# Optimization experiments

Hardware: AMD Instinct MI355X
Metric: run time of the kernel (lower is better)

Reference implementation:

```python
import jax, jax.numpy as jnp
import numpy as np

N_NODES = 500_000
N_EDGES = 16_000_000
N_LAYERS = 49
ALPHA = 0.3  # GCN2Conv alpha; beta = 1.0 (no theta/layer given)

# per-layer activation applied AFTER the conv (layer index 0-based)
_LEAKY = {1, 11, 21, 31, 41}
_SIG = {4, 14, 24, 34, 44}


def setup_inputs() -> dict:
    key = jax.random.key(0)
    k1, k2, k3 = jax.random.split(key, 3)
    x = jax.random.normal(k1, (N_NODES, 1), dtype=jnp.float32)
    adj = jax.random.randint(k2, (2, N_EDGES), 0, N_NODES, dtype=jnp.int64)
    # 49 scalar (1x1) layer weights
    w = jax.random.normal(k3, (N_LAYERS,), dtype=jnp.float32) * 0.1
    return {"input": x, "w": w, "adj": adj}


def _gcn_norm(adj, n):
    # add self-loops, symmetric normalization D^-1/2 (A+I) D^-1/2
    loops = jnp.arange(n, dtype=adj.dtype)
    src = jnp.concatenate([adj[0], loops])
    dst = jnp.concatenate([adj[1], loops])
    deg = jax.ops.segment_sum(jnp.ones(src.shape[0], jnp.float32), dst, num_segments=n)
    dis = 1.0 / jnp.sqrt(deg)  # deg >= 1 due to self-loops
    ew = dis[src] * dis[dst]
    return src, dst, ew


def reference(input, w, adj):
    n = input.shape[0]
    x0 = input.astype(jnp.float32)
    src, dst, ew = _gcn_norm(adj, n)
    ewc = ew[:, None]  # [E+N, 1]

    def gcn2(x, wl):
        h = jax.ops.segment_sum(ewc * x[src], dst, num_segments=n)  # A_hat @ x
        comb = (1.0 - ALPHA) * h + ALPHA * x0                       # residual mix
        return comb * wl                                            # 1x1 weight, beta=1

    x = x0
    for i in range(N_LAYERS):
        y = gcn2(x, w[i])
        if i == 0:
            x = y  # no activation after gcn1
        elif i == N_LAYERS - 1:
            x = n * jax.nn.sigmoid(y)  # CustomSigmoid: len(x) * sigmoid(x)
        elif i in _LEAKY:
            x = jax.nn.leaky_relu(y, 0.01)
        elif i in _SIG:
            x = jax.nn.sigmoid(y)
        else:
            x = jax.nn.relu(y)
        # dropout(p=0.0) is identity
    return jnp.squeeze(x, 1).astype(jnp.int64)
```

## Files before the change

### kernel.cpp

```cpp
#include <hip/hip_runtime.h>
#include <math.h>

#define NN 500000
#define NE 16000000
#define NBKT 1954
#define PB 40960
#define NPB_BLOCKS ((NE + PB - 1) / PB)

__global__ __launch_bounds__(256) void hist_kernel(const int4* __restrict__ dst4,
                                                   int* __restrict__ bcnt) {
    __shared__ int lh[NBKT];
    for (int i = threadIdx.x; i < NBKT; i += 256) lh[i] = 0;
    __syncthreads();
    long base4 = (long)blockIdx.x * (PB / 4);
    for (int k = 0; k < PB / 4; k += 256) {
        long i4 = base4 + k + threadIdx.x;
        if (i4 < NE / 4) {
            int4 d = dst4[i4];
            atomicAdd(&lh[d.x >> 8], 1);
            atomicAdd(&lh[d.y >> 8], 1);
            atomicAdd(&lh[d.z >> 8], 1);
            atomicAdd(&lh[d.w >> 8], 1);
        }
    }
    __syncthreads();
    for (int i = threadIdx.x; i < NBKT; i += 256) {
        int c = lh[i];
        if (c) atomicAdd(&bcnt[i], c);
    }
}

__global__ __launch_bounds__(256) void scan_buckets(int* __restrict__ bcnt,
                                                    int* __restrict__ bbase) {
    __shared__ int sh[256];
    __shared__ int carry_sh;
    if (threadIdx.x == 0) carry_sh = 0;
    __syncthreads();
    for (int base = 0; base < NBKT; base += 256) {
        int i = base + threadIdx.x;
        int v = (i < NBKT) ? bcnt[i] : 0;
        sh[threadIdx.x] = v;
        __syncthreads();
        for (int off = 1; off < 256; off <<= 1) {
            int t = (threadIdx.x >= off) ? sh[threadIdx.x - off] : 0;
            __syncthreads();
            sh[threadIdx.x] += t;
            __syncthreads();
        }
        int incl = sh[threadIdx.x];
        int c = carry_sh;
        __syncthreads();
        if (i < NBKT) {
            int ex = c + incl - v;
            bbase[i] = ex;
            bcnt[i] = ex;
        }
        if (threadIdx.x == 255) carry_sh = c + incl;
        __syncthreads();
    }
    if (threadIdx.x == 0) bbase[NBKT] = NE;
}

__global__ __launch_bounds__(256) void partition_kernel(const int* __restrict__ src,
                                                        const int* __restrict__ dst,
                                                        int* __restrict__ bcur,
                                                        int* __restrict__ ebuf) {
    __shared__ int lh[NBKT];
    for (int i = threadIdx.x; i < NBKT; i += 256) lh[i] = 0;
    __syncthreads();
    long base = (long)blockIdx.x * PB;
    for (int k = 0; k < PB; k += 256) {
        long e = base + k + threadIdx.x;
        if (e < NE) atomicAdd(&lh[dst[e] >> 8], 1);
    }
    __syncthreads();
    for (int i = threadIdx.x; i < NBKT; i += 256) {
        int c = lh[i];
        if (c) lh[i] = atomicAdd(&bcur[i], c);
    }
    __syncthreads();
    for (int k = 0; k < PB; k += 256) {
        long e = base + k + threadIdx.x;
        if (e < NE) {
            int d = dst[e];
            int pos = atomicAdd(&lh[d >> 8], 1);
            ebuf[pos] = ((d & 255) << 19) | src[e];
        }
    }
}

__global__ __launch_bounds__(256) void bucket_deg(const int* __restrict__ bbase,
                                                  const int* __restrict__ ebuf,
                                                  float* __restrict__ dis) {
    __shared__ int cnt[256];
    int b = blockIdx.x;
    int ebase = bbase[b];
    int nb = bbase[b + 1] - ebase;
    cnt[threadIdx.x] = 0;
    __syncthreads();
    for (int i = threadIdx.x; i < nb; i += 256)
        atomicAdd(&cnt[ebuf[ebase + i] >> 19], 1);
    __syncthreads();
    int v = b * 256 + threadIdx.x;
    if (v < NN) dis[v] = rsqrtf((float)(cnt[threadIdx.x] + 1));
}

__global__ void init_z(const float* __restrict__ x0, const float* __restrict__ dis,
                       float* __restrict__ z) {
    int i = blockIdx.x * 256 + threadIdx.x;
    if (i < NN) z[i] = x0[i] * dis[i];
}

__global__ __launch_bounds__(256) void layer_kernel(
        const int* __restrict__ bbase, const int* __restrict__ ebuf,
        const float* __restrict__ zin, const float* __restrict__ dis,
        const float* __restrict__ x0, const float* __restrict__ w,
        int li, int act, float* __restrict__ zout, int* __restrict__ out) {
    __shared__ float h[256];
    int b = blockIdx.x;
    int ebase = bbase[b];
    int nb = bbase[b + 1] - ebase;
    h[threadIdx.x] = 0.f;
    __syncthreads();
    for (int i = threadIdx.x; i < nb; i += 256) {
        int e = ebuf[ebase + i];
        atomicAdd(&h[e >> 19], zin[e & 0x7FFFF]);
    }
    __syncthreads();
    int v = b * 256 + threadIdx.x;
    if (v >= NN) return;
    float s = h[threadIdx.x] + zin[v];
    float hh = dis[v] * s;
    float comb = 0.7f * hh + 0.3f * x0[v];
    float y = comb * w[li];
    if (act == 4) {
        float sg = 1.f / (1.f + expf(-y));
        out[v] = (int)(500000.f * sg);
        return;
    }
    float r;
    if (act == 0)      r = y;
    else if (act == 1) r = fmaxf(y, 0.f);
    else if (act == 2) r = (y > 0.f) ? y : 0.01f * y;
    else               r = 1.f / (1.f + expf(-y));
    zout[v] = dis[v] * r;
}

extern "C" void kernel_launch(void* const* d_in, const int* in_sizes, int n_in,
                              void* d_out, int out_size, void* d_ws, size_t ws_size,
                              hipStream_t stream) {
    const float* x0  = (const float*)d_in[0];
    const float* w   = (const float*)d_in[1];
    const int*   adj = (const int*)d_in[2];
    const int*   src = adj;
    const int*   dst = adj + NE;
    int* out = (int*)d_out;

    uintptr_t p = (uintptr_t)d_ws;
    auto alloc = [&](size_t bytes) -> void* {
        p = (p + 255) & ~(uintptr_t)255;
        void* r = (void*)p;
        p += bytes;
        return r;
    };
    float* dis   = (float*)alloc((size_t)NN * 4);
    float* z0    = (float*)alloc((size_t)NN * 4);
    float* z1    = (float*)alloc((size_t)NN * 4);
    int*   bcnt  = (int*)alloc((size_t)NBKT * 4);
    int*   bbase = (int*)alloc((size_t)(NBKT + 1) * 4);
    int*   csr   = (int*)alloc((size_t)NE * 4);
    (void)ws_size;

    hipMemsetAsync(bcnt, 0, (size_t)NBKT * 4, stream);

    hist_kernel<<<NPB_BLOCKS, 256, 0, stream>>>((const int4*)dst, bcnt);
    scan_buckets<<<1, 256, 0, stream>>>(bcnt, bbase);
    partition_kernel<<<NPB_BLOCKS, 256, 0, stream>>>(src, dst, bcnt, csr);
    bucket_deg<<<NBKT, 256, 0, stream>>>(bbase, csr, dis);
    init_z<<<(NN + 255) / 256, 256, 0, stream>>>(x0, dis, z0);

    float* zbuf[2] = {z0, z1};
    for (int i = 0; i < 49; i++) {
        int act;
        if (i == 0)            act = 0;
        else if (i == 48)      act = 4;
        else if (i % 10 == 1)  act = 2;
        else if (i % 10 == 4)  act = 3;
        else                   act = 1;
        layer_kernel<<<NBKT, 256, 0, stream>>>(bbase, csr, zbuf[i & 1], dis, x0, w,
                                               i, act, zbuf[(i + 1) & 1], out);
    }
}
```

Measured before the change: 4.941 ms.

## Two-level partition of edges by dst supertile and src cell for gather locality

Edges are now first partitioned by destination into 8192-node supertiles, then within each supertile sorted by source cell (1024-node groups), so gathers of zin within a block hit nearby addresses. Each layer is split into an accumulate kernel, where 16 chunks per supertile reduce into an 8192-entry shared histogram and flush via global atomics, and a finalize kernel that applies the activation and clears the accumulator. This aims to improve cache locality of the random src gathers and to use larger shared tiles. In exchange it adds an extra sort pass, global float atomics, and a second launch per layer.

```diff
diff --git a/kernel.cpp b/kernel.cpp
--- a/kernel.cpp
+++ b/kernel.cpp
@@ -3,42 +3,131 @@
 
 #define NN 500000
 #define NE 16000000
-#define NBKT 1954
-#define PB 40960
-#define NPB_BLOCKS ((NE + PB - 1) / PB)
-
-__global__ __launch_bounds__(256) void hist_kernel(const int4* __restrict__ dst4,
-                                                   int* __restrict__ bcnt) {
-    __shared__ int lh[NBKT];
-    for (int i = threadIdx.x; i < NBKT; i += 256) lh[i] = 0;
-    __syncthreads();
-    long base4 = (long)blockIdx.x * (PB / 4);
-    for (int k = 0; k < PB / 4; k += 256) {
+#define ST 62
+#define STB 8192
+#define NG 489
+#define PBA 16384
+#define NBA ((NE/4 + PBA/4 - 1) / (PBA/4))
+#define SUBB 16
+#define NBB (ST * SUBB)
+#define CHUNKS 16
+#define NBACC (ST * CHUNKS)
+
+__global__ __launch_bounds__(256) void histA(const int4* __restrict__ dst4,
+                                             int* __restrict__ bcntA) {
+    __shared__ int lh[ST];
+    if (threadIdx.x < ST) lh[threadIdx.x] = 0;
+    __syncthreads();
+    long base4 = (long)blockIdx.x * (PBA / 4);
+    for (int k = 0; k < PBA / 4; k += 256) {
         long i4 = base4 + k + threadIdx.x;
         if (i4 < NE / 4) {
             int4 d = dst4[i4];
-            atomicAdd(&lh[d.x >> 8], 1);
-            atomicAdd(&lh[d.y >> 8], 1);
-            atomicAdd(&lh[d.z >> 8], 1);
-            atomicAdd(&lh[d.w >> 8], 1);
-        }
-    }
-    __syncthreads();
-    for (int i = threadIdx.x; i < NBKT; i += 256) {
-        int c = lh[i];
-        if (c) atomicAdd(&bcnt[i], c);
-    }
-}
-
-__global__ __launch_bounds__(256) void scan_buckets(int* __restrict__ bcnt,
-                                                    int* __restrict__ bbase) {
+            atomicAdd(&lh[d.x >> 13], 1);
+            atomicAdd(&lh[d.y >> 13], 1);
+            atomicAdd(&lh[d.z >> 13], 1);
+            atomicAdd(&lh[d.w >> 13], 1);
+        }
+    }
+    __syncthreads();
+    if (threadIdx.x < ST) {
+        int c = lh[threadIdx.x];
+        if (c) atomicAdd(&bcntA[threadIdx.x], c);
+    }
+}
+
+__global__ void scanA(const int* __restrict__ bcntA, int* __restrict__ regBase,
+                      int* __restrict__ curA) {
+    int i = threadIdx.x;
+    int v = (i < ST) ? bcntA[i] : 0;
+    int incl = v;
+    for (int off = 1; off < 64; off <<= 1) {
+        int t = __shfl_up(incl, off);
+        if (i >= off) incl += t;
+    }
+    if (i < ST) { regBase[i] = incl - v; curA[i] = incl - v; }
+    if (i == 63) regBase[ST] = incl;
+}
+
+__global__ __launch_bounds__(256) void scatterA(const int4* __restrict__ src4,
+                                                const int4* __restrict__ dst4,
+                                                int* __restrict__ curA,
+                                                unsigned* __restrict__ tmp) {
+    __shared__ int lh[ST];
+    if (threadIdx.x < ST) lh[threadIdx.x] = 0;
+    __syncthreads();
+    long base4 = (long)blockIdx.x * (PBA / 4);
+    for (int k = 0; k < PBA / 4; k += 256) {
+        long i4 = base4 + k + threadIdx.x;
+        if (i4 < NE / 4) {
+            int4 d = dst4[i4];
+            atomicAdd(&lh[d.x >> 13], 1);
+            atomicAdd(&lh[d.y >> 13], 1);
+            atomicAdd(&lh[d.z >> 13], 1);
+            atomicAdd(&lh[d.w >> 13], 1);
+        }
+    }
+    __syncthreads();
+    if (threadIdx.x < ST) {
+        int c = lh[threadIdx.x];
+        if (c) lh[threadIdx.x] = atomicAdd(&curA[threadIdx.x], c);
+    }
+    __syncthreads();
+    for (int k = 0; k < PBA / 4; k += 256) {
+        long i4 = base4 + k + threadIdx.x;
+        if (i4 < NE / 4) {
+            int4 d = dst4[i4];
+            int4 s = src4[i4];
+            int p;
+            p = atomicAdd(&lh[d.x >> 13], 1); tmp[p] = ((unsigned)(d.x & 8191) << 19) | (unsigned)s.x;
+            p = atomicAdd(&lh[d.y >> 13], 1); tmp[p] = ((unsigned)(d.y & 8191) << 19) | (unsigned)s.y;
+            p = atomicAdd(&lh[d.z >> 13], 1); tmp[p] = ((unsigned)(d.z & 8191) << 19) | (unsigned)s.z;
+            p = atomicAdd(&lh[d.w >> 13], 1); tmp[p] = ((unsigned)(d.w & 8191) << 19) | (unsigned)s.w;
+        }
+    }
+}
+
+__global__ __launch_bounds__(256) void histB(const unsigned* __restrict__ tmp,
+                                             const int* __restrict__ regBase,
+                                             int* __restrict__ cellCnt,
+                                             int* __restrict__ deg) {
+    __shared__ int gh[NG];
+    __shared__ int dh[STB];
+    int st = blockIdx.x >> 4, sb = blockIdx.x & 15;
+    int base = regBase[st];
+    int len = regBase[st + 1] - base;
+    int beg = base + (int)((long)len * sb / SUBB);
+    int end = base + (int)((long)len * (sb + 1) / SUBB);
+    for (int i = threadIdx.x; i < NG; i += 256) gh[i] = 0;
+    for (int i = threadIdx.x; i < STB; i += 256) dh[i] = 0;
+    __syncthreads();
+    for (int i = beg + threadIdx.x; i < end; i += 256) {
+        unsigned e = tmp[i];
+        atomicAdd(&gh[(e & 0x7FFFFu) >> 10], 1);
+        atomicAdd(&dh[e >> 19], 1);
+    }
+    __syncthreads();
+    for (int i = threadIdx.x; i < NG; i += 256) {
+        int c = gh[i];
+        if (c) atomicAdd(&cellCnt[st * NG + i], c);
+    }
+    for (int i = threadIdx.x; i < STB; i += 256) {
+        int c = dh[i];
+        if (c) atomicAdd(&deg[st * STB + i], c);
+    }
+}
+
+__global__ __launch_bounds__(256) void scanB(const int* __restrict__ regBase,
+                                             const int* __restrict__ cellCnt,
+                                             int* __restrict__ cellCur) {
     __shared__ int sh[256];
     __shared__ int carry_sh;
-    if (threadIdx.x == 0) carry_sh = 0;
-    __syncthreads();
-    for (int base = 0; base < NBKT; base += 256) {
+    int st = blockIdx.x;
+    if (threadIdx.x == 0) carry_sh = regBase[st];
+    __syncthreads();
+    for (int base = 0; base < NG; base += 256) {
         int i = base + threadIdx.x;
-        int v = (i < NBKT) ? bcnt[i] : 0;
+        int v = (i < NG) ? cellCnt[st * NG + i] : 0;
         sh[threadIdx.x] = v;
         __syncthreads();
         for (int off = 1; off < 256; off <<= 1) {
@@ -50,86 +139,86 @@
         int incl = sh[threadIdx.x];
         int c = carry_sh;
         __syncthreads();
-        if (i < NBKT) {
-            int ex = c + incl - v;
-            bbase[i] = ex;
-            bcnt[i] = ex;
-        }
+        if (i < NG) cellCur[st * NG + i] = c + incl - v;
         if (threadIdx.x == 255) carry_sh = c + incl;
         __syncthreads();
     }
-    if (threadIdx.x == 0) bbase[NBKT] = NE;
-}
-
-__global__ __launch_bounds__(256) void partition_kernel(const int* __restrict__ src,
-                                                        const int* __restrict__ dst,
-                                                        int* __restrict__ bcur,
-                                                        int* __restrict__ ebuf) {
-    __shared__ int lh[NBKT];
-    for (int i = threadIdx.x; i < NBKT; i += 256) lh[i] = 0;
-    __syncthreads();
-    long base = (long)blockIdx.x * PB;
-    for (int k = 0; k < PB; k += 256) {
-        long e = base + k + threadIdx.x;
-        if (e < NE) atomicAdd(&lh[dst[e] >> 8], 1);
-    }
-    __syncthreads();
-    for (int i = threadIdx.x; i < NBKT; i += 256) {
-        int c = lh[i];
-        if (c) lh[i] = atomicAdd(&bcur[i], c);
-    }
-    __syncthreads();
-    for (int k = 0; k < PB; k += 256) {
-        long e = base + k + threadIdx.x;
-        if (e < NE) {
-            int d = dst[e];
-            int pos = atomicAdd(&lh[d >> 8], 1);
-            ebuf[pos] = ((d & 255) << 19) | src[e];
-        }
-    }
-}
-
-__global__ __launch_bounds__(256) void bucket_deg(const int* __restrict__ bbase,
-                                                  const int* __restrict__ ebuf,
-                                                  float* __restrict__ dis) {
-    __shared__ int cnt[256];
-    int b = blockIdx.x;
-    int ebase = bbase[b];
-    int nb = bbase[b + 1] - ebase;
-    cnt[threadIdx.x] = 0;
-    __syncthreads();
-    for (int i = threadIdx.x; i < nb; i += 256)
-        atomicAdd(&cnt[ebuf[ebase + i] >> 19], 1);
-    __syncthreads();
-    int v = b * 256 + threadIdx.x;
-    if (v < NN) dis[v] = rsqrtf((float)(cnt[threadIdx.x] + 1));
-}
-
-__global__ void init_z(const float* __restrict__ x0, const float* __restrict__ dis,
-                       float* __restrict__ z) {
-    int i = blockIdx.x * 256 + threadIdx.x;
-    if (i < NN) z[i] = x0[i] * dis[i];
-}
-
-__global__ __launch_bounds__(256) void layer_kernel(
-        const int* __restrict__ bbase, const int* __restrict__ ebuf,
-        const float* __restrict__ zin, const float* __restrict__ dis,
-        const float* __restrict__ x0, const float* __restrict__ w,
-        int li, int act, float* __restrict__ zout, int* __restrict__ out) {
-    __shared__ float h[256];
-    int b = blockIdx.x;
-    int ebase = bbase[b];
-    int nb = bbase[b + 1] - ebase;
-    h[threadIdx.x] = 0.f;
-    __syncthreads();
-    for (int i = threadIdx.x; i < nb; i += 256) {
-        int e = ebuf[ebase + i];
-        atomicAdd(&h[e >> 19], zin[e & 0x7FFFF]);
-    }
-    __syncthreads();
-    int v = b * 256 + threadIdx.x;
+}
+
+__global__ __launch_bounds__(256) void scatterB(const unsigned* __restrict__ tmp,
+                                                const int* __restrict__ regBase,
+                                                int* __restrict__ cellCur,
+                                                unsigned* __restrict__ ebuf) {
+    __shared__ int gh[NG];
+    int st = blockIdx.x >> 4, sb = blockIdx.x & 15;
+    int base = regBase[st];
+    int len = regBase[st + 1] - base;
+    int beg = base + (int)((long)len * sb / SUBB);
+    int end = base + (int)((long)len * (sb + 1) / SUBB);
+    for (int i = threadIdx.x; i < NG; i += 256) gh[i] = 0;
+    __syncthreads();
+    for (int i = beg + threadIdx.x; i < end; i += 256)
+        atomicAdd(&gh[(tmp[i] & 0x7FFFFu) >> 10], 1);
+    __syncthreads();
+    for (int i = threadIdx.x; i < NG; i += 256) {
+        int c = gh[i];
+        if (c) gh[i] = atomicAdd(&cellCur[st * NG + i], c);
+    }
+    __syncthreads();
+    for (int i = beg + threadIdx.x; i < end; i += 256) {
+        unsigned e = tmp[i];
+        int pos = atomicAdd(&gh[(e & 0x7FFFFu) >> 10], 1);
+        ebuf[pos] = e;
+    }
+}
+
+__global__ void disz(const int* __restrict__ deg, const float* __restrict__ x0,
+                     float* __restrict__ dis, float* __restrict__ z0) {
+    int v = blockIdx.x * 256 + threadIdx.x;
+    if (v < NN) {
+        float f = rsqrtf((float)(deg[v] + 1));
+        dis[v] = f;
+        z0[v] = x0[v] * f;
+    }
+}
+
+__global__ __launch_bounds__(512) void accum(const unsigned* __restrict__ ebuf,
+                                             const int* __restrict__ regBase,
+                                             const float* __restrict__ zin,
+                                             float* __restrict__ hglob) {
+    __shared__ float h[STB];
+    int st = blockIdx.x >> 4, c = blockIdx.x & 15;
+    int base = regBase[st];
+    int len = regBase[st + 1] - base;
+    int beg = base + (int)((long)len * c / CHUNKS);
+    int end = base + (int)((long)len * (c + 1) / CHUNKS);
+    for (int j = threadIdx.x; j < STB; j += 512) h[j] = 0.f;
+    __syncthreads();
+    #pragma unroll 4
+    for (int i = beg + threadIdx.x; i < end; i += 512) {
+        unsigned e = ebuf[i];
+        atomicAdd(&h[e >> 19], zin[e & 0x7FFFFu]);
+    }
+    __syncthreads();
+    for (int j = threadIdx.x; j < STB; j += 512) {
+        float v = h[j];
+        if (v != 0.f) atomicAdd(&hglob[st * STB + j], v);
+    }
+}
+
+__global__ __launch_bounds__(256) void finalize(float* __restrict__ hglob,
+                                                const float* __restrict__ zin,
+                                                const float* __restrict__ dis,
+                                                const float* __restrict__ x0,
+                                                const float* __restrict__ w,
+                                                int li, int act,
+                                                float* __restrict__ zout,
+                                                int* __restrict__ out) {
+    int v = blockIdx.x * 256 + threadIdx.x;
     if (v >= NN) return;
-    float s = h[threadIdx.x] + zin[v];
+    float hv = hglob[v];
+    hglob[v] = 0.f;
+    float s = hv + zin[v];
     float hh = dis[v] * s;
     float comb = 0.7f * hh + 0.3f * x0[v];
     float y = comb * w[li];
@@ -163,21 +252,32 @@
         p += bytes;
         return r;
     };
-    float* dis   = (float*)alloc((size_t)NN * 4);
-    float* z0    = (float*)alloc((size_t)NN * 4);
-    float* z1    = (float*)alloc((size_t)NN * 4);
-    int*   bcnt  = (int*)alloc((size_t)NBKT * 4);
-    int*   bbase = (int*)alloc((size_t)(NBKT + 1) * 4);
-    int*   csr   = (int*)alloc((size_t)NE * 4);
+    float*    dis     = (float*)alloc((size_t)NN * 4);
+    float*    z0      = (float*)alloc((size_t)NN * 4);
+    float*    z1      = (float*)alloc((size_t)NN * 4);
+    int*      deg     = (int*)alloc((size_t)NN * 4);
+    float*    hglob   = (float*)alloc((size_t)ST * STB * 4);
+    int*      bcntA   = (int*)alloc((size_t)ST * 4);
+    int*      regBase = (int*)alloc((size_t)(ST + 1) * 4);
+    int*      curA    = (int*)alloc((size_t)ST * 4);
+    int*      cellCnt = (int*)alloc((size_t)ST * NG * 4);
+    int*      cellCur = (int*)alloc((size_t)ST * NG * 4);
+    unsigned* tmp     = (unsigned*)alloc((size_t)NE * 4);
+    unsigned* ebuf    = (unsigned*)alloc((size_t)NE * 4);
     (void)ws_size;
 
-    hipMemsetAsync(bcnt, 0, (size_t)NBKT * 4, stream);
-
-    hist_kernel<<<NPB_BLOCKS, 256, 0, stream>>>((const int4*)dst, bcnt);
-    scan_buckets<<<1, 256, 0, stream>>>(bcnt, bbase);
-    partition_kernel<<<NPB_BLOCKS, 256, 0, stream>>>(src, dst, bcnt, csr);
-    bucket_deg<<<NBKT, 256, 0, stream>>>(bbase, csr, dis);
-    init_z<<<(NN + 255) / 256, 256, 0, stream>>>(x0, dis, z0);
+    hipMemsetAsync(bcntA, 0, (size_t)ST * 4, stream);
+    hipMemsetAsync(cellCnt, 0, (size_t)ST * NG * 4, stream);
+    hipMemsetAsync(deg, 0, (size_t)NN * 4, stream);
+    hipMemsetAsync(hglob, 0, (size_t)ST * STB * 4, stream);
+
+    histA<<<NBA, 256, 0, stream>>>((const int4*)dst, bcntA);
+    scanA<<<1, 64, 0, stream>>>(bcntA, regBase, curA);
+    scatterA<<<NBA, 256, 0, stream>>>((const int4*)src, (const int4*)dst, curA, tmp);
+    histB<<<NBB, 256, 0, stream>>>(tmp, regBase, cellCnt, deg);
+    scanB<<<ST, 256, 0, stream>>>(regBase, cellCnt, cellCur);
+    scatterB<<<NBB, 256, 0, stream>>>(tmp, regBase, cellCur, ebuf);
+    disz<<<(NN + 255) / 256, 256, 0, stream>>>(deg, x0, dis, z0);
 
     float* zbuf[2] = {z0, z1};
     for (int i = 0; i < 49; i++) {
@@ -187,7 +287,8 @@
         else if (i % 10 == 1)  act = 2;
         else if (i % 10 == 4)  act = 3;
         else                   act = 1;
-        layer_kernel<<<NBKT, 256, 0, stream>>>(bbase, csr, zbuf[i & 1], dis, x0, w,
-                                               i, act, zbuf[(i + 1) & 1], out);
-    }
-}
+        accum<<<NBACC, 512, 0, stream>>>(ebuf, regBase, zbuf[i & 1], hglob);
+        finalize<<<(NN + 255) / 256, 256, 0, stream>>>(hglob, zbuf[i & 1], dis, x0, w,
+                                                       i, act, zbuf[(i + 1) & 1], out);
+    }
+}
```

Result: slower. 5.451 ms (+10.3%).
